# Kernel tuning notes

Hardware: AMD Instinct MI355X
Metric: run time of the kernel (lower is better)

The kernel has to match this reference:

```python
import jax, jax.numpy as jnp
import numpy as np

# Multi-scale feature pyramid (H, W) per level, standard Deformable-DETR for ~800x800 input
SHAPES = [(100, 100), (50, 50), (25, 25), (13, 13)]
D = 256      # d_model
NH = 8       # n_heads
NL = 4       # n_levels
NP = 4       # n_points
HD = D // NH # head_dim = 32
B = 2
S = sum(h * w for h, w in SHAPES)  # 13294
Lq = S  # encoder-style: one query per multi-scale token


def setup_inputs() -> dict:
    key = jax.random.key(0)
    ks = jax.random.split(key, 11)
    return {
        "query": jax.random.normal(ks[0], (B, Lq, D), jnp.float32),
        "reference_points": jax.random.uniform(ks[1], (B, Lq, NL, 2), jnp.float32),
        "value": jax.random.normal(ks[2], (B, S, D), jnp.float32),
        "W_val": jax.random.normal(ks[3], (D, D), jnp.float32) * 0.02,
        "b_val": jnp.zeros((D,), jnp.float32),
        "W_off": jax.random.normal(ks[4], (D, NH * NL * NP * 2), jnp.float32) * 0.01,
        "b_off": jax.random.normal(ks[5], (NH * NL * NP * 2,), jnp.float32) * 0.5,
        "W_attn": jax.random.normal(ks[6], (D, NH * NL * NP), jnp.float32) * 0.02,
        "b_attn": jnp.zeros((NH * NL * NP,), jnp.float32),
        "W_out": jax.random.normal(ks[7], (D, D), jnp.float32) * 0.02,
        "b_out": jnp.zeros((D,), jnp.float32),
    }


def _bilinear_sample(valf, x, y, H, W):
    """grid_sample(mode=bilinear, padding_mode=zeros, align_corners=False).
    valf: [N, H*W, C] flattened feature map; x, y: [N, P] pixel-space coords
    (already converted via x = loc_x*W - 0.5). Returns [N, P, C].
    """
    x0 = jnp.floor(x); y0 = jnp.floor(y)
    x1 = x0 + 1.0;     y1 = y0 + 1.0
    wx1 = x - x0; wx0 = 1.0 - wx1
    wy1 = y - y0; wy0 = 1.0 - wy1

    def corner(xi, yi, w):
        inb = (xi >= 0) & (xi <= W - 1) & (yi >= 0) & (yi <= H - 1)
        xi_c = jnp.clip(xi, 0, W - 1).astype(jnp.int32)
        yi_c = jnp.clip(yi, 0, H - 1).astype(jnp.int32)
        idx = yi_c * W + xi_c                                   # [N, P]
        v = jnp.take_along_axis(valf, idx[..., None], axis=1)   # [N, P, C]
        return v * (w * inb.astype(valf.dtype))[..., None]

    return (corner(x0, y0, wx0 * wy0) + corner(x1, y0, wx1 * wy0)
            + corner(x0, y1, wx0 * wy1) + corner(x1, y1, wx1 * wy1))


def reference(query, reference_points, value, W_val, b_val, W_off, b_off,
              W_attn, b_attn, W_out, b_out):
    Bq, L, _ = query.shape
    # value projection, split into heads: [B, S, NH, HD]
    val = (value @ W_val + b_val).reshape(Bq, S, NH, HD)
    # sampling offsets and attention weights from query
    offsets = (query @ W_off + b_off).reshape(Bq, L, NH, NL, NP, 2)
    w = (query @ W_attn + b_attn).reshape(Bq, L, NH, NL * NP)
    w = jax.nn.softmax(w, axis=-1).reshape(Bq, L, NH, NL, NP)
    # normalize offsets by (W, H) per level; 2D reference points path
    offset_norm = jnp.array([[wd, h] for h, wd in SHAPES], jnp.float32)  # [NL, 2]
    locs = (reference_points[:, :, None, :, None, :]
            + offsets / offset_norm[None, None, None, :, None, :])       # [B,L,NH,NL,NP,2]

    splits = [h * wd for h, wd in SHAPES]
    starts = np.concatenate([[0], np.cumsum(splits)])
    out_acc = jnp.zeros((Bq, L, NH, HD), query.dtype)
    for lvl, (H, W) in enumerate(SHAPES):
        vl = val[:, starts[lvl]:starts[lvl + 1]]                 # [B, HW, NH, HD]
        vl = vl.transpose(0, 2, 1, 3).reshape(Bq * NH, H * W, HD)
        loc = locs[:, :, :, lvl].transpose(0, 2, 1, 3, 4).reshape(Bq * NH, L * NP, 2)
        x = loc[..., 0] * W - 0.5   # align_corners=False pixel coords
        y = loc[..., 1] * H - 0.5
        s = _bilinear_sample(vl, x, y, H, W).reshape(Bq, NH, L, NP, HD)
        wl = w[:, :, :, lvl].transpose(0, 2, 1, 3)               # [B, NH, L, NP]
        out_acc = out_acc + jnp.einsum('bhqpd,bhqp->bqhd', s, wl)
    out = out_acc.reshape(Bq, L, NH * HD)
    return out @ W_out + b_out
```

## Files before the change

### kernel.cpp

```cpp
#include <hip/hip_runtime.h>
#include <hip/hip_bf16.h>
#include <math.h>

#define B_    2
#define NH_   8
#define NL_   4
#define NP_   4
#define HD_   32
#define S_    13294
#define L_    13294
#define M_    26588

__device__ __constant__ int c_H[NL_]     = {100, 50, 25, 13};
__device__ __constant__ int c_W[NL_]     = {100, 50, 25, 13};
__device__ __constant__ int c_start[NL_] = {0, 10000, 12500, 13125};

typedef __attribute__((ext_vector_type(8))) _Float16 f16x8;
typedef __attribute__((ext_vector_type(2))) _Float16 f16x2;
typedef __attribute__((ext_vector_type(4))) float    float4v;

__device__ __forceinline__ unsigned short f2h(float f) {
    _Float16 h = (_Float16)f;
    return __builtin_bit_cast(unsigned short, h);
}
__device__ __forceinline__ float h2f(unsigned short u) {
    _Float16 h = __builtin_bit_cast(_Float16, u);
    return (float)h;
}
__device__ __forceinline__ f16x2 pkrtz(float a, float b) {
    return __builtin_bit_cast(f16x2, __builtin_amdgcn_cvt_pkrtz(a, b));
}

__global__ __launch_bounds__(256) void prep_weights(
    const float* __restrict__ W_val, const float* __restrict__ W_off,
    const float* __restrict__ W_attn, const float* __restrict__ b_off,
    const float* __restrict__ b_attn, const float* __restrict__ W_out,
    unsigned short* __restrict__ wt_val, unsigned short* __restrict__ wt_oa,
    unsigned short* __restrict__ wt_out, float* __restrict__ bias_oa)
{
    int i = blockIdx.x * 256 + threadIdx.x;
    if (i < 65536) {
        int n = i >> 8, k = i & 255;
        wt_val[i] = f2h(W_val[k * 256 + n]);
    } else if (i < 65536 + 98304) {
        int j = i - 65536;
        int n = j >> 8, k = j & 255;
        float v = (n < 256) ? W_off[k * 256 + n] : W_attn[k * 128 + (n - 256)];
        wt_oa[j] = f2h(v);
    } else if (i < 65536 + 98304 + 65536) {
        int j = i - 163840;
        int n = j >> 8, k = j & 255;
        wt_out[j] = f2h(W_out[k * 256 + n]);
    } else if (i < 229376 + 384) {
        int j = i - 229376;
        bias_oa[j] = (j < 256) ? b_off[j] : b_attn[j - 256];
    }
}

template<int N, int OUT, bool AF32>
__device__ __forceinline__ void gemm_body(
    const void* __restrict__ Av,
    const unsigned short* __restrict__ WT,
    const float* __restrict__ bias,
    void* __restrict__ Cv,
    unsigned short (* __restrict__ As)[64][40])
{
    constexpr int NT = N / 64;

    const int tid  = threadIdx.x;
    const int lane = tid & 63;
    const int wave = tid >> 6;
    const int rowBase = blockIdx.x * 64;
    const int wcol = wave * (N / 4);

    const int ar   = tid >> 2;
    const int ako  = (tid & 3) * 8;
    const int grow = rowBase + ar;
    const int fr   = lane & 15;
    const int fk   = (lane >> 4) * 8;

    float4v acc[4][NT] = {};

    const unsigned short* bbase[NT];
#pragma unroll
    for (int t = 0; t < NT; ++t)
        bbase[t] = WT + (size_t)(wcol + t * 16 + fr) * 256 + fk;

    f16x8 curB[NT], nxtB[NT];
    float4 ra0, ra1;
    f16x8  rah;

    auto loadA = [&](int k0) {
        if constexpr (AF32) {
            const float* A = (const float*)Av;
            if (grow < M_) {
                ra0 = *reinterpret_cast<const float4*>(A + (size_t)grow * 256 + k0 + ako);
                ra1 = *reinterpret_cast<const float4*>(A + (size_t)grow * 256 + k0 + ako + 4);
            } else { ra0 = make_float4(0.f,0.f,0.f,0.f); ra1 = ra0; }
        } else {
            const unsigned short* A = (const unsigned short*)Av;
            if (grow < M_)
                rah = *reinterpret_cast<const f16x8*>(A + (size_t)grow * 256 + k0 + ako);
            else
                rah = f16x8{};
        }
    };
    auto storeA = [&](int buf) {
        f16x8 s;
        if constexpr (AF32) {
            f16x2 p0 = pkrtz(ra0.x, ra0.y);
            f16x2 p1 = pkrtz(ra0.z, ra0.w);
            f16x2 p2 = pkrtz(ra1.x, ra1.y);
            f16x2 p3 = pkrtz(ra1.z, ra1.w);
            s[0]=p0[0]; s[1]=p0[1]; s[2]=p1[0]; s[3]=p1[1];
            s[4]=p2[0]; s[5]=p2[1]; s[6]=p3[0]; s[7]=p3[1];
        } else {
            s = rah;
        }
        *reinterpret_cast<f16x8*>(&As[buf][ar][ako]) = s;
    };
    auto loadB = [&](f16x8* dst, int k0) {
#pragma unroll
        for (int t = 0; t < NT; ++t)
            dst[t] = *reinterpret_cast<const f16x8*>(bbase[t] + k0);
    };

    loadA(0);
    loadB(curB, 0);
    storeA(0);
    loadA(32);

#pragma unroll
    for (int it = 0; it < 8; ++it) {
        __syncthreads();
        f16x8 af[4];
#pragma unroll
        for (int t = 0; t < 4; ++t)
            af[t] = *reinterpret_cast<const f16x8*>(&As[it & 1][t * 16 + fr][fk]);
        if (it < 7) {
            storeA((it + 1) & 1);
            if (it < 6) loadA((it + 2) * 32);
            loadB(nxtB, (it + 1) * 32);
        }
#pragma unroll
        for (int mt = 0; mt < 4; ++mt)
#pragma unroll
            for (int nt = 0; nt < NT; ++nt)
                acc[mt][nt] = __builtin_amdgcn_mfma_f32_16x16x32_f16(
                    af[mt], curB[nt], acc[mt][nt], 0, 0, 0);
        if (it < 7) {
#pragma unroll
            for (int t = 0; t < NT; ++t) curB[t] = nxtB[t];
        }
    }

    const int dn  = lane & 15;
    const int dm0 = (lane >> 4) * 4;
#pragma unroll
    for (int mt = 0; mt < 4; ++mt) {
#pragma unroll
        for (int nt = 0; nt < NT; ++nt) {
            const int col = wcol + nt * 16 + dn;
            const float bv = bias[col];
#pragma unroll
            for (int r = 0; r < 4; ++r) {
                const int row = rowBase + mt * 16 + dm0 + r;
                if (row < M_) {
                    const float v = acc[mt][nt][r] + bv;
                    if constexpr (OUT == 0)
                        ((unsigned short*)Cv)[(size_t)row * 256 + col] = f2h(v);
                    else if constexpr (OUT == 1)
                        ((unsigned short*)Cv)[(size_t)row * 384 + col] = f2h(v);
                    else
                        ((float*)Cv)[(size_t)row * 256 + col] = v;
                }
            }
        }
    }
}

__global__ __launch_bounds__(256) void gemm_vq(
    const float* __restrict__ value, const float* __restrict__ query,
    const unsigned short* __restrict__ wt_val, const unsigned short* __restrict__ wt_oa,
    const float* __restrict__ b_val, const float* __restrict__ bias_oa,
    unsigned short* __restrict__ val_f16, unsigned short* __restrict__ oa_f16)
{
    __shared__ unsigned short As[2][64][40];
    if (blockIdx.y == 0)
        gemm_body<256, 0, true>(value, wt_val, b_val, val_f16, As);
    else
        gemm_body<384, 1, true>(query, wt_oa, bias_oa, oa_f16, As);
}

__global__ __launch_bounds__(256) void gemm_out3(
    const unsigned short* __restrict__ Af16,
    const unsigned short* __restrict__ WT,
    const float* __restrict__ bias, float* __restrict__ C)
{
    __shared__ unsigned short As[2][64][40];
    gemm_body<256, 2, false>(Af16, WT, bias, C, As);
}

__global__ __launch_bounds__(256, 8) void deform_sample_v6(
    const unsigned short* __restrict__ val,
    const float* __restrict__ refp,
    const unsigned short* __restrict__ oa,
    unsigned short* __restrict__ acc)
{
    __shared__ int sP[4][1088];

    const int tid  = threadIdx.x;
    const int wave = tid >> 6;
    const int l    = tid & 63;

    const int q   = l >> 5;
    const int h   = (l >> 2) & 7;
    const int lvl = l & 3;
    const int qw  = blockIdx.x * 8 + wave * 2 + q;
    const int bq  = min(qw, M_ - 1);

    int* __restrict__ sw = sP[wave];

    {
        const int2 lgi = *reinterpret_cast<const int2*>(
            oa + (size_t)bq * 384 + 256 + h * 16 + lvl * 4);
        const f16x2 lp0 = __builtin_bit_cast(f16x2, lgi.x);
        const f16x2 lp1 = __builtin_bit_cast(f16x2, lgi.y);
        float lg[4] = { (float)lp0[0], (float)lp0[1], (float)lp1[0], (float)lp1[1] };

        float m = fmaxf(fmaxf(lg[0], lg[1]), fmaxf(lg[2], lg[3]));
        m = fmaxf(m, __shfl_xor(m, 1));
        m = fmaxf(m, __shfl_xor(m, 2));

        float e[4], s = 0.f;
#pragma unroll
        for (int j = 0; j < 4; ++j) { e[j] = __expf(lg[j] - m); s += e[j]; }
        s += __shfl_xor(s, 1);
        s += __shfl_xor(s, 2);
        const float rinv = 1.f / s;

        const int Wi = c_W[lvl], Hi = c_H[lvl], st = c_start[lvl];
        const float2 rxy = *reinterpret_cast<const float2*>(
            refp + ((size_t)bq * NL_ + lvl) * 2);
        const f16x8 off8 = *reinterpret_cast<const f16x8*>(
            oa + (size_t)bq * 384 + h * 32 + lvl * 8);

#pragma unroll
        for (int j = 0; j < 4; ++j) {
            const float wgt = e[j] * rinv;
            const float x = rxy.x * (float)Wi + (float)off8[2 * j]     - 0.5f;
            const float y = rxy.y * (float)Hi + (float)off8[2 * j + 1] - 0.5f;
            const float x0f = floorf(x), y0f = floorf(y);
            const int   x0 = (int)x0f,   y0 = (int)y0f;
            const float wx1 = x - x0f, wx0 = 1.f - wx1;
            const float wy1 = y - y0f, wy0 = 1.f - wy1;

            const int   cx[4] = {x0, x0 + 1, x0,     x0 + 1};
            const int   cy[4] = {y0, y0,     y0 + 1, y0 + 1};
            const float cw[4] = {wx0 * wy0, wx1 * wy0, wx0 * wy1, wx1 * wy1};
            const int base = q * 544 + (lvl * 4 + j) * 34 + h;
#pragma unroll
            for (int c = 0; c < 4; ++c) {
                const bool inb = (cx[c] >= 0) & (cx[c] < Wi) & (cy[c] >= 0) & (cy[c] < Hi);
                const int xi = min(max(cx[c], 0), Wi - 1);
                const int yi = min(max(cy[c], 0), Hi - 1);
                const int idx = st + yi * Wi + xi;
                const unsigned short wh = f2h(inb ? wgt * cw[c] : 0.f);
                sw[base + c * 8] = idx | ((int)wh << 16);
            }
        }
    }

    const int d4 = lvl;
    const unsigned short* vb = val + (size_t)(bq / L_) * S_ * 256 + h * 32 + d4 * 8;
    const int rbase = q * 544 + h;

    f16x2 A0{}, A1{}, A2{}, A3{};
#pragma unroll 8
    for (int i = 0; i < 64; ++i) {
        const int lp = i >> 2;
        const int c  = i & 3;
        const int pk = sw[rbase + lp * 34 + c * 8];
        const unsigned wb = (unsigned)pk >> 16;
        const f16x2 w2 = __builtin_bit_cast(f16x2, (wb << 16) | wb);
        const int4 u = *reinterpret_cast<const int4*>(
            vb + (size_t)((unsigned)pk & 0xffffu) * 256);
        A0 += w2 * __builtin_bit_cast(f16x2, u.x);
        A1 += w2 * __builtin_bit_cast(f16x2, u.y);
        A2 += w2 * __builtin_bit_cast(f16x2, u.z);
        A3 += w2 * __builtin_bit_cast(f16x2, u.w);
    }
    if (qw < M_) {
        int4 o;
        o.x = __builtin_bit_cast(int, A0);
        o.y = __builtin_bit_cast(int, A1);
        o.z = __builtin_bit_cast(int, A2);
        o.w = __builtin_bit_cast(int, A3);
        *reinterpret_cast<int4*>(acc + (size_t)qw * 256 + h * 32 + d4 * 8) = o;
    }
}

extern "C" void kernel_launch(void* const* d_in, const int* in_sizes, int n_in,
                              void* d_out, int out_size, void* d_ws, size_t ws_size,
                              hipStream_t stream) {
    const float* query  = (const float*)d_in[0];
    const float* refp   = (const float*)d_in[1];
    const float* value  = (const float*)d_in[2];
    const float* W_val  = (const float*)d_in[3];
    const float* b_val  = (const float*)d_in[4];
    const float* W_off  = (const float*)d_in[5];
    const float* b_off  = (const float*)d_in[6];
    const float* W_attn = (const float*)d_in[7];
    const float* b_attn = (const float*)d_in[8];
    const float* W_out  = (const float*)d_in[9];
    const float* b_out  = (const float*)d_in[10];
    float* out = (float*)d_out;

    char* ws = (char*)d_ws;
    const size_t mb = (size_t)M_ * 256;
    unsigned short* val_f16 = (unsigned short*)ws;  ws += mb * 2;
    unsigned short* acc_f16 = (unsigned short*)ws;  ws += mb * 2;
    unsigned short* oa_f16  = (unsigned short*)ws;  ws += (size_t)M_ * 384 * 2;
    unsigned short* wt_val  = (unsigned short*)ws;  ws += 65536 * 2;
    unsigned short* wt_oa   = (unsigned short*)ws;  ws += 98304 * 2;
    unsigned short* wt_out  = (unsigned short*)ws;  ws += 65536 * 2;
    float*          bias_oa = (float*)ws;           ws += 384 * 4;

    dim3 blk(256);

    prep_weights<<<dim3(898), blk, 0, stream>>>(
        W_val, W_off, W_attn, b_off, b_attn, W_out, wt_val, wt_oa, wt_out, bias_oa);

    gemm_vq<<<dim3((M_ + 63) / 64, 2), blk, 0, stream>>>(
        value, query, wt_val, wt_oa, b_val, bias_oa, val_f16, oa_f16);

    deform_sample_v6<<<dim3((M_ + 7) / 8), blk, 0, stream>>>(val_f16, refp, oa_f16, acc_f16);

    gemm_out3<<<dim3((M_ + 63) / 64), blk, 0, stream>>>(acc_f16, wt_out, b_out, out);
}
```

Baseline: 208.7 us.

## Fuse output projection GEMM into deformable sampling kernel via LDS and MFMA

```diff
diff --git a/kernel.cpp b/kernel.cpp
--- a/kernel.cpp
+++ b/kernel.cpp
@@ -192,22 +192,16 @@
         gemm_body<384, 1, true>(query, wt_oa, bias_oa, oa_f16, As);
 }
 
-__global__ __launch_bounds__(256) void gemm_out3(
-    const unsigned short* __restrict__ Af16,
-    const unsigned short* __restrict__ WT,
-    const float* __restrict__ bias, float* __restrict__ C)
-{
-    __shared__ unsigned short As[2][64][40];
-    gemm_body<256, 2, false>(Af16, WT, bias, C, As);
-}
-
-__global__ __launch_bounds__(256, 8) void deform_sample_v6(
+__global__ __launch_bounds__(256, 7) void deform_out_v9(
     const unsigned short* __restrict__ val,
     const float* __restrict__ refp,
     const unsigned short* __restrict__ oa,
-    unsigned short* __restrict__ acc)
+    const unsigned short* __restrict__ wt_out,
+    const float* __restrict__ b_out,
+    float* __restrict__ out)
 {
     __shared__ int sP[4][1088];
+    __shared__ unsigned short sAcc[8][272];
 
     const int tid  = threadIdx.x;
     const int wave = tid >> 6;
@@ -290,13 +284,54 @@
         A2 += w2 * __builtin_bit_cast(f16x2, u.z);
         A3 += w2 * __builtin_bit_cast(f16x2, u.w);
     }
-    if (qw < M_) {
+    {
         int4 o;
         o.x = __builtin_bit_cast(int, A0);
         o.y = __builtin_bit_cast(int, A1);
         o.z = __builtin_bit_cast(int, A2);
         o.w = __builtin_bit_cast(int, A3);
-        *reinterpret_cast<int4*>(acc + (size_t)qw * 256 + h * 32 + d4 * 8) = o;
+        *reinterpret_cast<int4*>(&sAcc[wave * 2 + q][h * 32 + d4 * 8]) = o;
+    }
+    __syncthreads();
+
+    {
+        const int fr   = l & 15;
+        const int fk   = (l >> 4) * 8;
+        const int wcol = wave * 64;
+
+        const unsigned short* bb[4];
+#pragma unroll
+        for (int t = 0; t < 4; ++t)
+            bb[t] = wt_out + (size_t)(wcol + t * 16 + fr) * 256 + fk;
+
+        float4v oacc[4] = {};
+#pragma unroll
+        for (int k0 = 0; k0 < 256; k0 += 32) {
+            const f16x8 af = *reinterpret_cast<const f16x8*>(&sAcc[fr & 7][k0 + fk]);
+            f16x8 bf[4];
+#pragma unroll
+            for (int t = 0; t < 4; ++t)
+                bf[t] = *reinterpret_cast<const f16x8*>(bb[t] + k0);
+#pragma unroll
+            for (int t = 0; t < 4; ++t)
+                oacc[t] = __builtin_amdgcn_mfma_f32_16x16x32_f16(
+                    af, bf[t], oacc[t], 0, 0, 0);
+        }
+
+        const int dn  = l & 15;
+        const int dm0 = (l >> 4) * 4;
+        const int q0  = blockIdx.x * 8;
+#pragma unroll
+        for (int t = 0; t < 4; ++t) {
+            const int col = wcol + t * 16 + dn;
+            const float bv = b_out[col];
+#pragma unroll
+            for (int r = 0; r < 4; ++r) {
+                const int row = dm0 + r;
+                if (row < 8 && q0 + row < M_)
+                    out[(size_t)(q0 + row) * 256 + col] = oacc[t][r] + bv;
+            }
+        }
     }
 }
 
@@ -325,6 +360,7 @@
     unsigned short* wt_oa   = (unsigned short*)ws;  ws += 98304 * 2;
     unsigned short* wt_out  = (unsigned short*)ws;  ws += 65536 * 2;
     float*          bias_oa = (float*)ws;           ws += 384 * 4;
+    (void)acc_f16;
 
     dim3 blk(256);
 
@@ -334,7 +370,6 @@
     gemm_vq<<<dim3((M_ + 63) / 64, 2), blk, 0, stream>>>(
         value, query, wt_val, wt_oa, b_val, bias_oa, val_f16, oa_f16);
 
-    deform_sample_v6<<<dim3((M_ + 7) / 8), blk, 0, stream>>>(val_f16, refp, oa_f16, acc_f16);
-
-    gemm_out3<<<dim3((M_ + 63) / 64), blk, 0, stream>>>(acc_f16, wt_out, b_out, out);
-}
+    deform_out_v9<<<dim3((M_ + 7) / 8), blk, 0, stream>>>(
+        val_f16, refp, oa_f16, wt_out, b_out, out);
+}
```

Measured after the change: 232.0 us. 1.11x slower.

## Load GEMM A fragments directly from global memory, dropping LDS staging and barriers

Applied to the files above, without the earlier changes.

```diff
diff --git a/kernel.cpp b/kernel.cpp
--- a/kernel.cpp
+++ b/kernel.cpp
@@ -58,12 +58,11 @@
 }
 
 template<int N, int OUT, bool AF32>
-__device__ __forceinline__ void gemm_body(
+__device__ __forceinline__ void gemm_nb(
     const void* __restrict__ Av,
     const unsigned short* __restrict__ WT,
     const float* __restrict__ bias,
-    void* __restrict__ Cv,
-    unsigned short (* __restrict__ As)[64][40])
+    void* __restrict__ Cv)
 {
     constexpr int NT = N / 64;
 
@@ -73,11 +72,8 @@
     const int rowBase = blockIdx.x * 64;
     const int wcol = wave * (N / 4);
 
-    const int ar   = tid >> 2;
-    const int ako  = (tid & 3) * 8;
-    const int grow = rowBase + ar;
-    const int fr   = lane & 15;
-    const int fk   = (lane >> 4) * 8;
+    const int fr = lane & 15;
+    const int fk = (lane >> 4) * 8;
 
     float4v acc[4][NT] = {};
 
@@ -86,72 +82,46 @@
     for (int t = 0; t < NT; ++t)
         bbase[t] = WT + (size_t)(wcol + t * 16 + fr) * 256 + fk;
 
-    f16x8 curB[NT], nxtB[NT];
-    float4 ra0, ra1;
-    f16x8  rah;
-
-    auto loadA = [&](int k0) {
-        if constexpr (AF32) {
-            const float* A = (const float*)Av;
-            if (grow < M_) {
-                ra0 = *reinterpret_cast<const float4*>(A + (size_t)grow * 256 + k0 + ako);
-                ra1 = *reinterpret_cast<const float4*>(A + (size_t)grow * 256 + k0 + ako + 4);
-            } else { ra0 = make_float4(0.f,0.f,0.f,0.f); ra1 = ra0; }
-        } else {
-            const unsigned short* A = (const unsigned short*)Av;
-            if (grow < M_)
-                rah = *reinterpret_cast<const f16x8*>(A + (size_t)grow * 256 + k0 + ako);
-            else
-                rah = f16x8{};
+    const float*          a32[4];
+    const unsigned short* a16[4];
+#pragma unroll
+    for (int mt = 0; mt < 4; ++mt) {
+        const int row = min(rowBase + mt * 16 + fr, M_ - 1);
+        if constexpr (AF32) a32[mt] = (const float*)Av + (size_t)row * 256 + fk;
+        else                a16[mt] = (const unsigned short*)Av + (size_t)row * 256 + fk;
+    }
+
+#pragma unroll
+    for (int it = 0; it < 8; ++it) {
+        const int k0 = it * 32;
+        f16x8 af[4];
+#pragma unroll
+        for (int mt = 0; mt < 4; ++mt) {
+            if constexpr (AF32) {
+                const float4 r0 = *reinterpret_cast<const float4*>(a32[mt] + k0);
+                const float4 r1 = *reinterpret_cast<const float4*>(a32[mt] + k0 + 4);
+                const f16x2 p0 = pkrtz(r0.x, r0.y);
+                const f16x2 p1 = pkrtz(r0.z, r0.w);
+                const f16x2 p2 = pkrtz(r1.x, r1.y);
+                const f16x2 p3 = pkrtz(r1.z, r1.w);
+                f16x8 s;
+                s[0]=p0[0]; s[1]=p0[1]; s[2]=p1[0]; s[3]=p1[1];
+                s[4]=p2[0]; s[5]=p2[1]; s[6]=p3[0]; s[7]=p3[1];
+                af[mt] = s;
+            } else {
+                af[mt] = *reinterpret_cast<const f16x8*>(a16[mt] + k0);
+            }
         }
-    };
-    auto storeA = [&](int buf) {
-        f16x8 s;
-        if constexpr (AF32) {
-            f16x2 p0 = pkrtz(ra0.x, ra0.y);
-            f16x2 p1 = pkrtz(ra0.z, ra0.w);
-            f16x2 p2 = pkrtz(ra1.x, ra1.y);
-            f16x2 p3 = pkrtz(ra1.z, ra1.w);
-            s[0]=p0[0]; s[1]=p0[1]; s[2]=p1[0]; s[3]=p1[1];
-            s[4]=p2[0]; s[5]=p2[1]; s[6]=p3[0]; s[7]=p3[1];
-        } else {
-            s = rah;
-        }
-        *reinterpret_cast<f16x8*>(&As[buf][ar][ako]) = s;
-    };
-    auto loadB = [&](f16x8* dst, int k0) {
+        f16x8 bf[NT];
 #pragma unroll
         for (int t = 0; t < NT; ++t)
-            dst[t] = *reinterpret_cast<const f16x8*>(bbase[t] + k0);
-    };
-
-    loadA(0);
-    loadB(curB, 0);
-    storeA(0);
-    loadA(32);
-
-#pragma unroll
-    for (int it = 0; it < 8; ++it) {
-        __syncthreads();
-        f16x8 af[4];
-#pragma unroll
-        for (int t = 0; t < 4; ++t)
-            af[t] = *reinterpret_cast<const f16x8*>(&As[it & 1][t * 16 + fr][fk]);
-        if (it < 7) {
-            storeA((it + 1) & 1);
-            if (it < 6) loadA((it + 2) * 32);
-            loadB(nxtB, (it + 1) * 32);
-        }
+            bf[t] = *reinterpret_cast<const f16x8*>(bbase[t] + k0);
 #pragma unroll
         for (int mt = 0; mt < 4; ++mt)
 #pragma unroll
             for (int nt = 0; nt < NT; ++nt)
                 acc[mt][nt] = __builtin_amdgcn_mfma_f32_16x16x32_f16(
-                    af[mt], curB[nt], acc[mt][nt], 0, 0, 0);
-        if (it < 7) {
-#pragma unroll
-            for (int t = 0; t < NT; ++t) curB[t] = nxtB[t];
-        }
+                    af[mt], bf[nt], acc[mt][nt], 0, 0, 0);
     }
 
     const int dn  = lane & 15;
@@ -185,11 +155,10 @@
     const float* __restrict__ b_val, const float* __restrict__ bias_oa,
     unsigned short* __restrict__ val_f16, unsigned short* __restrict__ oa_f16)
 {
-    __shared__ unsigned short As[2][64][40];
     if (blockIdx.y == 0)
-        gemm_body<256, 0, true>(value, wt_val, b_val, val_f16, As);
+        gemm_nb<256, 0, true>(value, wt_val, b_val, val_f16);
     else
-        gemm_body<384, 1, true>(query, wt_oa, bias_oa, oa_f16, As);
+        gemm_nb<384, 1, true>(query, wt_oa, bias_oa, oa_f16);
 }
 
 __global__ __launch_bounds__(256) void gemm_out3(
@@ -197,8 +166,7 @@
     const unsigned short* __restrict__ WT,
     const float* __restrict__ bias, float* __restrict__ C)
 {
-    __shared__ unsigned short As[2][64][40];
-    gemm_body<256, 2, false>(Af16, WT, bias, C, As);
+    gemm_nb<256, 2, false>(Af16, WT, bias, C);
 }
 
 __global__ __launch_bounds__(256, 8) void deform_sample_v6(
```

After: 236.9 us. +13.5%, slower.
